# Kernel tuning notes

Hardware: AMD Instinct MI355X
Metric: run time of the kernel (lower is better)

Reference implementation:

```python
import jax, jax.numpy as jnp
import numpy as np

M_DIM = 1024
H_DIM = 1024
NEG = -1e9


def setup_inputs() -> dict:
    key = jax.random.key(0)
    ks = jax.random.split(key, 9)
    B, S = 4, 2048
    q = jax.random.normal(ks[0], (B, S, M_DIM), dtype=jnp.float32)
    k = jax.random.normal(ks[1], (B, S, M_DIM), dtype=jnp.float32)
    v = jax.random.normal(ks[2], (B, S, M_DIM), dtype=jnp.float32)
    attention_mask = jnp.ones((B, S), dtype=jnp.int32)
    sc = 1.0 / np.sqrt(M_DIM)
    Wq_w = jax.random.normal(ks[3], (H_DIM, M_DIM), dtype=jnp.float32) * sc
    Wq_b = jnp.zeros((H_DIM,), dtype=jnp.float32)
    Wk_w = jax.random.normal(ks[4], (H_DIM, M_DIM), dtype=jnp.float32) * sc
    Wk_b = jnp.zeros((H_DIM,), dtype=jnp.float32)
    Wv_w = jax.random.normal(ks[5], (H_DIM, M_DIM), dtype=jnp.float32) * sc
    Wv_b = jnp.zeros((H_DIM,), dtype=jnp.float32)
    return {"q": q, "k": k, "v": v, "attention_mask": attention_mask,
            "Wq_w": Wq_w, "Wq_b": Wq_b, "Wk_w": Wk_w, "Wk_b": Wk_b,
            "Wv_w": Wv_w, "Wv_b": Wv_b}


def reference(q, k, v, attention_mask, Wq_w, Wq_b, Wk_w, Wk_b, Wv_w, Wv_b):
    # Linear projections (torch Linear: x @ W.T + b)
    qh = jnp.einsum('bsm,hm->bsh', q, Wq_w) + Wq_b
    kh = jnp.einsum('bsm,hm->bsh', k, Wk_w) + Wk_b
    vh = jnp.einsum('bsm,hm->bsh', v, Wv_w) + Wv_b
    # Scaled dot-product scores: [B, Sq, Sk]
    scores = jnp.einsum('bqh,bkh->bqk', qh, kh) / jnp.sqrt(jnp.float32(H_DIM))
    # Padding mask: attention_mask [B, Sk] -> [B, 1, Sk]
    pad = attention_mask.astype(bool)[:, None, :]
    scores = jnp.where(pad, scores, NEG)
    # Causal mask (apply_mask=True)
    Sq, Sk = scores.shape[1], scores.shape[2]
    causal = jnp.tril(jnp.ones((Sq, Sk), dtype=bool))
    scores = jnp.where(causal[None, :, :], scores, NEG)
    attn = jax.nn.softmax(scores, axis=-1)
    out = jnp.einsum('bqk,bkh->bqh', attn, vh)
    # dropout is identity in eval mode
    return out
```

## Files before the change

### kernel.cpp

```cpp
#include <hip/hip_runtime.h>
#include <stdint.h>


typedef __attribute__((ext_vector_type(8))) short s8v;
typedef __attribute__((ext_vector_type(4))) float f4v;

__device__ __forceinline__ unsigned short f2bf(float f) {
    union { float f; unsigned u; } v; v.f = f;
    unsigned u = v.u;
    u = u + 0x7fffu + ((u >> 16) & 1u);
    return (unsigned short)(u >> 16);
}

__device__ __forceinline__ void gld_lds16(const void* gptr, void* lptr) {
    __builtin_amdgcn_global_load_lds(
        (const __attribute__((address_space(1))) unsigned int*)(uintptr_t)gptr,
        (__attribute__((address_space(3))) unsigned int*)(unsigned int)(uintptr_t)lptr,
        16, 0, 0);
}

__global__ __launch_bounds__(256) void convert_all(
    const float* __restrict__ q, const float* __restrict__ k, const float* __restrict__ v,
    const float* __restrict__ wq, const float* __restrict__ wk, const float* __restrict__ wv,
    unsigned short* __restrict__ qb, unsigned short* __restrict__ kb, unsigned short* __restrict__ vb,
    unsigned short* __restrict__ wqb, unsigned short* __restrict__ wkb, unsigned short* __restrict__ wvb,
    float* __restrict__ l)
{
    int b = blockIdx.x;
    if (b >= 27648) {
        int li = (b - 27648) * 256 + threadIdx.x;
        l[li] = 0.f;
        return;
    }
    const float* src; unsigned short* dst; int blk;
    if (b < 8192)       { src = q;  dst = qb;  blk = b; }
    else if (b < 16384) { src = k;  dst = kb;  blk = b - 8192; }
    else if (b < 24576) { src = v;  dst = vb;  blk = b - 16384; }
    else if (b < 25600) { src = wq; dst = wqb; blk = b - 24576; }
    else if (b < 26624) { src = wk; dst = wkb; blk = b - 25600; }
    else                { src = wv; dst = wvb; blk = b - 26624; }
    size_t idx = (size_t)blk * 1024 + (size_t)threadIdx.x * 4;
    float4 f = *(const float4*)(src + idx);
    ushort4 o = make_ushort4(f2bf(f.x), f2bf(f.y), f2bf(f.z), f2bf(f.w));
    *(ushort4*)(dst + idx) = o;
}

__device__ __forceinline__ void gemm_tiles(
    const unsigned short* __restrict__ A, int lda,
    const unsigned short* __restrict__ Bt, int ldb,
    int m0, int n0, int kTiles,
    unsigned short* As, unsigned short* Bs,
    f4v acc[4][4])
{
    const int t    = threadIdx.x;
    const int lane = t & 63;
    const int wave = t >> 6;
    const int wm   = (wave >> 1) * 64;
    const int wn   = (wave & 1) * 64;
    const int l15  = lane & 15;
    const int quad = lane >> 4;

    const int c0 = t, c1 = t + 256;
    unsigned short* As0 = As + (c0 & ~63) * 8;
    unsigned short* As1 = As + (c1 & ~63) * 8;
    unsigned short* Bs0 = Bs + (c0 & ~63) * 8;
    unsigned short* Bs1 = Bs + (c1 & ~63) * 8;
    const unsigned short* Ag0 = A  + (size_t)(m0 + (c0 >> 2)) * lda + (c0 & 3) * 8;
    const unsigned short* Ag1 = A  + (size_t)(m0 + (c1 >> 2)) * lda + (c1 & 3) * 8;
    const unsigned short* Bg0 = Bt + (size_t)(n0 + (c0 >> 2)) * ldb + (c0 & 3) * 8;
    const unsigned short* Bg1 = Bt + (size_t)(n0 + (c1 >> 2)) * ldb + (c1 & 3) * 8;

    const unsigned short* a_base = As + quad * 8;
    const unsigned short* b_base = Bs + quad * 8;

    gld_lds16(Ag0, As0);
    gld_lds16(Ag1, As1);
    gld_lds16(Bg0, Bs0);
    gld_lds16(Bg1, Bs1);

    for (int kt = 0; kt < kTiles; ++kt) {
        __syncthreads();
        Ag0 += 32; Ag1 += 32; Bg0 += 32; Bg1 += 32;
        if (kt + 1 < kTiles) {
            const int nb = ((kt + 1) & 1) * 4096;
            gld_lds16(Ag0, As0 + nb);
            gld_lds16(Ag1, As1 + nb);
            gld_lds16(Bg0, Bs0 + nb);
            gld_lds16(Bg1, Bs1 + nb);
        }
        const int cb = (kt & 1) * 4096;
        s8v af[4], bf[4];
        #pragma unroll
        for (int i = 0; i < 4; ++i)
            af[i] = *(const s8v*)(a_base + cb + (wm + i * 16 + l15) * 32);
        #pragma unroll
        for (int j = 0; j < 4; ++j)
            bf[j] = *(const s8v*)(b_base + cb + (wn + j * 16 + l15) * 32);
        #pragma unroll
        for (int i = 0; i < 4; ++i)
            #pragma unroll
            for (int j = 0; j < 4; ++j)
                acc[i][j] = __builtin_amdgcn_mfma_f32_16x16x32_bf16(af[i], bf[j], acc[i][j], 0, 0, 0);
    }
}

#define ACC_INIT  f4v acc[4][4]; { f4v z = {0.f,0.f,0.f,0.f}; \
    _Pragma("unroll") for (int i = 0; i < 4; ++i) \
    _Pragma("unroll") for (int j = 0; j < 4; ++j) acc[i][j] = z; }

#define LANE_VARS \
    const int lane = threadIdx.x & 63; const int wave = threadIdx.x >> 6; \
    const int wm = (wave >> 1) * 64;  const int wn = (wave & 1) * 64; \
    const int l15 = lane & 15;        const int quad = lane >> 4;

__global__ __launch_bounds__(256) void proj_kernel(
    const unsigned short* __restrict__ qb, const unsigned short* __restrict__ wqb,
    const float* __restrict__ bq, unsigned short* __restrict__ QH,
    const unsigned short* __restrict__ kb, const unsigned short* __restrict__ wkb,
    const float* __restrict__ bk, unsigned short* __restrict__ KH,
    const unsigned short* __restrict__ vb, const unsigned short* __restrict__ wvb,
    const float* __restrict__ bv, unsigned short* __restrict__ VHT)
{
    const int z = blockIdx.z;
    const unsigned short* X; const unsigned short* W; const float* bias; unsigned short* Y;
    if (z == 0)      { X = qb; W = wqb; bias = bq; Y = QH; }
    else if (z == 1) { X = kb; W = wkb; bias = bk; Y = KH; }
    else             { X = vb; W = wvb; bias = bv; Y = VHT; }

    __shared__ __align__(16) unsigned short As[2 * 128 * 32];
    __shared__ __align__(16) unsigned short Bs[2 * 128 * 32];
    const int m0 = blockIdx.x * 128;
    const int n0 = blockIdx.y * 128;
    ACC_INIT;
    gemm_tiles(X, 1024, W, 1024, m0, n0, 32, As, Bs, acc);
    LANE_VARS;
    #pragma unroll
    for (int i = 0; i < 4; ++i) {
        int row = m0 + wm + i * 16 + quad * 4;
        #pragma unroll
        for (int j = 0; j < 4; ++j) {
            int col = n0 + wn + j * 16 + l15;
            float bvv = bias[col];
            if (z != 2) {
                #pragma unroll
                for (int r = 0; r < 4; ++r)
                    Y[(size_t)(row + r) * 1024 + col] = f2bf(acc[i][j][r] + bvv);
            } else {
                int bb = row >> 11;
                int s  = row & 2047;
                ushort4 o = make_ushort4(f2bf(acc[i][j][0] + bvv), f2bf(acc[i][j][1] + bvv),
                                         f2bf(acc[i][j][2] + bvv), f2bf(acc[i][j][3] + bvv));
                *(ushort4*)(Y + (size_t)bb * (1024 * 2048) + (size_t)col * 2048 + s) = o;
            }
        }
    }
}

__global__ __launch_bounds__(256) void score_kernel(
    const unsigned short* __restrict__ QH, const unsigned short* __restrict__ KH,
    const int* __restrict__ mask, unsigned short* __restrict__ P, float* __restrict__ lsum)
{
    const int b = blockIdx.y;
    int tq = blockIdx.x;
    int qt = 0;
    while ((qt + 1) * (qt + 2) / 2 <= tq) ++qt;
    const int kt = tq - qt * (qt + 1) / 2;

    __shared__ __align__(16) unsigned short As[2 * 128 * 32];
    __shared__ __align__(16) unsigned short Bs[2 * 128 * 32];
    const unsigned short* A  = QH + (size_t)b * 2048 * 1024;
    const unsigned short* Bt = KH + (size_t)b * 2048 * 1024;
    unsigned short* Pb = P + (size_t)b * 2048 * 2048;
    float* lb = lsum + b * 2048;
    const int* mb = mask + b * 2048;
    const int m0 = qt * 128, n0 = kt * 128;
    ACC_INIT;
    gemm_tiles(A, 1024, Bt, 1024, m0, n0, 32, As, Bs, acc);
    LANE_VARS;
    float rs[4][4];
    #pragma unroll
    for (int i = 0; i < 4; ++i)
        #pragma unroll
        for (int r = 0; r < 4; ++r) rs[i][r] = 0.f;
    #pragma unroll
    for (int i = 0; i < 4; ++i) {
        int qbase = m0 + wm + i * 16 + quad * 4;
        #pragma unroll
        for (int j = 0; j < 4; ++j) {
            int kg = n0 + wn + j * 16 + l15;
            int mv = mb[kg];
            #pragma unroll
            for (int r = 0; r < 4; ++r) {
                float s = acc[i][j][r] * 0.03125f;
                float p = (mv && (kg <= qbase + r)) ? __expf(s) : 0.f;
                Pb[(size_t)(qbase + r) * 2048 + kg] = f2bf(p);
                rs[i][r] += p;
            }
        }
    }
    #pragma unroll
    for (int i = 0; i < 4; ++i)
        #pragma unroll
        for (int r = 0; r < 4; ++r) {
            float v_ = rs[i][r];
            v_ += __shfl_xor(v_, 1);
            v_ += __shfl_xor(v_, 2);
            v_ += __shfl_xor(v_, 4);
            v_ += __shfl_xor(v_, 8);
            if (l15 == 0)
                atomicAdd(&lb[m0 + wm + i * 16 + quad * 4 + r], v_);
        }
}

__constant__ int pv_qt[24] = {15,15, 7,14,14,13,13, 6,12,12,11,11, 5,10,10, 9, 9, 4, 8, 8, 3, 2, 1, 0};
__constant__ int pv_ks[24] = { 0,32, 0, 0,30, 0,28, 0, 0,26, 0,24, 0, 0,22, 0,20, 0, 0,18, 0, 0, 0, 0};
__constant__ int pv_kc[24] = {32,32,32,30,30,28,28,28,26,26,24,24,24,22,22,20,20,20,18,18,16,12, 8, 4};

__global__ __launch_bounds__(256) void pv_kernel(
    const unsigned short* __restrict__ P, const unsigned short* __restrict__ VHT,
    const float* __restrict__ lsum, float* __restrict__ Out, float* __restrict__ Part)
{
    const int nt = blockIdx.x, y = blockIdx.y, b = blockIdx.z;
    const int qt = pv_qt[y], kstart = pv_ks[y], kcount = pv_kc[y];

    __shared__ __align__(16) unsigned short As[2 * 128 * 32];
    __shared__ __align__(16) unsigned short Bs[2 * 128 * 32];
    const unsigned short* A  = P   + (size_t)b * 2048 * 2048 + (size_t)kstart * 32;
    const unsigned short* Bt = VHT + (size_t)b * 1024 * 2048 + (size_t)kstart * 32;
    const float* lb = lsum + b * 2048;
    const int m0 = qt * 128, n0 = nt * 128;
    ACC_INIT;
    gemm_tiles(A, 2048, Bt, 2048, m0, n0, kcount, As, Bs, acc);
    LANE_VARS;
    float* dst; int rowoff;
    if (kstart == 0) { dst = Out  + (size_t)b * 2048 * 1024; rowoff = 0; }
    else             { dst = Part + (size_t)b * 1024 * 1024; rowoff = -1024; }
    #pragma unroll
    for (int i = 0; i < 4; ++i) {
        int q0 = m0 + wm + i * 16 + quad * 4;
        float inv[4];
        #pragma unroll
        for (int r = 0; r < 4; ++r) inv[r] = 1.0f / lb[q0 + r];
        #pragma unroll
        for (int j = 0; j < 4; ++j) {
            int h = n0 + wn + j * 16 + l15;
            #pragma unroll
            for (int r = 0; r < 4; ++r)
                dst[(size_t)(q0 + r + rowoff) * 1024 + h] = acc[i][j][r] * inv[r];
        }
    }
}

__global__ __launch_bounds__(256) void add_partial(
    float4* __restrict__ Out4, const float4* __restrict__ Part4)
{
    int i = blockIdx.x * 256 + threadIdx.x;
    int b = i >> 18;
    int rem = i & 262143;
    int oi = b * 524288 + 262144 + rem;
    float4 o = Out4[oi], p = Part4[i];
    o.x += p.x; o.y += p.y; o.z += p.z; o.w += p.w;
    Out4[oi] = o;
}

extern "C" void kernel_launch(void* const* d_in, const int* in_sizes, int n_in,
                              void* d_out, int out_size, void* d_ws, size_t ws_size,
                              hipStream_t stream)
{
    const float* q    = (const float*)d_in[0];
    const float* k    = (const float*)d_in[1];
    const float* v    = (const float*)d_in[2];
    const int*   mask = (const int*)d_in[3];
    const float* Wq   = (const float*)d_in[4];
    const float* bq   = (const float*)d_in[5];
    const float* Wk   = (const float*)d_in[6];
    const float* bk   = (const float*)d_in[7];
    const float* Wv   = (const float*)d_in[8];
    const float* bv   = (const float*)d_in[9];
    float* out = (float*)d_out;

    char* ws = (char*)d_ws;
    size_t off = 0;
    auto take = [&](size_t bytes) { char* p = ws + off; off += (bytes + 255) & ~(size_t)255; return p; };
    unsigned short* qb  = (unsigned short*)take(8192ull * 1024 * 2);
    unsigned short* kb  = (unsigned short*)take(8192ull * 1024 * 2);
    unsigned short* vb  = (unsigned short*)take(8192ull * 1024 * 2);
    unsigned short* wqb = (unsigned short*)take(1024ull * 1024 * 2);
    unsigned short* wkb = (unsigned short*)take(1024ull * 1024 * 2);
    unsigned short* wvb = (unsigned short*)take(1024ull * 1024 * 2);
    unsigned short* QH  = (unsigned short*)take(8192ull * 1024 * 2);
    unsigned short* KH  = (unsigned short*)take(8192ull * 1024 * 2);
    unsigned short* VHT = (unsigned short*)take(8192ull * 1024 * 2);
    unsigned short* P   = (unsigned short*)take(4ull * 2048 * 2048 * 2);
    float*          l   = (float*)take(4ull * 2048 * 4);
    float*          Part = (float*)qb;

    convert_all<<<27680, 256, 0, stream>>>(q, k, v, Wq, Wk, Wv,
                                           qb, kb, vb, wqb, wkb, wvb, l);
    proj_kernel<<<dim3(64, 8, 3), 256, 0, stream>>>(qb, wqb, bq, QH,
                                                    kb, wkb, bk, KH,
                                                    vb, wvb, bv, VHT);
    score_kernel<<<dim3(136, 4), 256, 0, stream>>>(QH, KH, mask, P, l);
    pv_kernel<<<dim3(8, 24, 4), 256, 0, stream>>>(P, VHT, l, out, Part);
    add_partial<<<4096, 256, 0, stream>>>((float4*)out, (const float4*)Part);
}
```

Before: 316.2 us.

## Replace split-K partial buffer with atomic accumulation and unroll GEMM double-buffer loop

The PV kernel's split-K blocks for the lower half of the query rows now atomically add into the output, which the convert kernel zeroes beforehand. This removes the Part buffer and the separate add_partial kernel launch. The shared GEMM loop is also manually unrolled by two with fixed buffer parities and 32-bit offsets, to cut per-iteration address arithmetic. In exchange, float atomics add contention on the output and make the summation order nondeterministic, and the unrolled loop assumes kTiles is even.

```diff
diff --git a/kernel.cpp b/kernel.cpp
--- a/kernel.cpp
+++ b/kernel.cpp
@@ -24,9 +24,16 @@
     const float* __restrict__ wq, const float* __restrict__ wk, const float* __restrict__ wv,
     unsigned short* __restrict__ qb, unsigned short* __restrict__ kb, unsigned short* __restrict__ vb,
     unsigned short* __restrict__ wqb, unsigned short* __restrict__ wkb, unsigned short* __restrict__ wvb,
-    float* __restrict__ l)
+    float* __restrict__ l, float4* __restrict__ Out4)
 {
     int b = blockIdx.x;
+    if (b >= 27680) {
+        int i = (b - 27680) * 256 + threadIdx.x;
+        int bb = i >> 18;
+        int rem = i & 262143;
+        Out4[bb * 524288 + 262144 + rem] = make_float4(0.f, 0.f, 0.f, 0.f);
+        return;
+    }
     if (b >= 27648) {
         int li = (b - 27648) * 256 + threadIdx.x;
         l[li] = 0.f;
@@ -65,42 +72,47 @@
     unsigned short* As1 = As + (c1 & ~63) * 8;
     unsigned short* Bs0 = Bs + (c0 & ~63) * 8;
     unsigned short* Bs1 = Bs + (c1 & ~63) * 8;
-    const unsigned short* Ag0 = A  + (size_t)(m0 + (c0 >> 2)) * lda + (c0 & 3) * 8;
-    const unsigned short* Ag1 = A  + (size_t)(m0 + (c1 >> 2)) * lda + (c1 & 3) * 8;
-    const unsigned short* Bg0 = Bt + (size_t)(n0 + (c0 >> 2)) * ldb + (c0 & 3) * 8;
-    const unsigned short* Bg1 = Bt + (size_t)(n0 + (c1 >> 2)) * ldb + (c1 & 3) * 8;
+    const unsigned aoff0 = (unsigned)(m0 + (c0 >> 2)) * lda + (c0 & 3) * 8;
+    const unsigned aoff1 = (unsigned)(m0 + (c1 >> 2)) * lda + (c1 & 3) * 8;
+    const unsigned boff0 = (unsigned)(n0 + (c0 >> 2)) * ldb + (c0 & 3) * 8;
+    const unsigned boff1 = (unsigned)(n0 + (c1 >> 2)) * ldb + (c1 & 3) * 8;
 
     const unsigned short* a_base = As + quad * 8;
     const unsigned short* b_base = Bs + quad * 8;
 
-    gld_lds16(Ag0, As0);
-    gld_lds16(Ag1, As1);
-    gld_lds16(Bg0, Bs0);
-    gld_lds16(Bg1, Bs1);
-
-    for (int kt = 0; kt < kTiles; ++kt) {
-        __syncthreads();
-        Ag0 += 32; Ag1 += 32; Bg0 += 32; Bg1 += 32;
-        if (kt + 1 < kTiles) {
-            const int nb = ((kt + 1) & 1) * 4096;
-            gld_lds16(Ag0, As0 + nb);
-            gld_lds16(Ag1, As1 + nb);
-            gld_lds16(Bg0, Bs0 + nb);
-            gld_lds16(Bg1, Bs1 + nb);
-        }
-        const int cb = (kt & 1) * 4096;
+    auto stage = [&](int kk, int par) {
+        const unsigned short* Au = A  + (size_t)kk * 32;
+        const unsigned short* Bu = Bt + (size_t)kk * 32;
+        const int pe = par * 4096;
+        gld_lds16(Au + aoff0, As0 + pe);
+        gld_lds16(Au + aoff1, As1 + pe);
+        gld_lds16(Bu + boff0, Bs0 + pe);
+        gld_lds16(Bu + boff1, Bs1 + pe);
+    };
+    auto compute = [&](int pe) {
         s8v af[4], bf[4];
         #pragma unroll
         for (int i = 0; i < 4; ++i)
-            af[i] = *(const s8v*)(a_base + cb + (wm + i * 16 + l15) * 32);
+            af[i] = *(const s8v*)(a_base + pe + (wm + i * 16 + l15) * 32);
         #pragma unroll
         for (int j = 0; j < 4; ++j)
-            bf[j] = *(const s8v*)(b_base + cb + (wn + j * 16 + l15) * 32);
+            bf[j] = *(const s8v*)(b_base + pe + (wn + j * 16 + l15) * 32);
         #pragma unroll
         for (int i = 0; i < 4; ++i)
             #pragma unroll
             for (int j = 0; j < 4; ++j)
                 acc[i][j] = __builtin_amdgcn_mfma_f32_16x16x32_bf16(af[i], bf[j], acc[i][j], 0, 0, 0);
+    };
+
+    stage(0, 0);
+    const int K2 = kTiles >> 1;
+    for (int k2 = 0; k2 < K2; ++k2) {
+        __syncthreads();
+        stage(2 * k2 + 1, 1);
+        compute(0);
+        __syncthreads();
+        if (k2 + 1 < K2) stage(2 * k2 + 2, 0);
+        compute(4096);
     }
 }
 
@@ -218,7 +230,7 @@
 
 __global__ __launch_bounds__(256) void pv_kernel(
     const unsigned short* __restrict__ P, const unsigned short* __restrict__ VHT,
-    const float* __restrict__ lsum, float* __restrict__ Out, float* __restrict__ Part)
+    const float* __restrict__ lsum, float* __restrict__ Out)
 {
     const int nt = blockIdx.x, y = blockIdx.y, b = blockIdx.z;
     const int qt = pv_qt[y], kstart = pv_ks[y], kcount = pv_kc[y];
@@ -228,13 +240,12 @@
     const unsigned short* A  = P   + (size_t)b * 2048 * 2048 + (size_t)kstart * 32;
     const unsigned short* Bt = VHT + (size_t)b * 1024 * 2048 + (size_t)kstart * 32;
     const float* lb = lsum + b * 2048;
+    float* Ob = Out + (size_t)b * 2048 * 1024;
     const int m0 = qt * 128, n0 = nt * 128;
     ACC_INIT;
     gemm_tiles(A, 2048, Bt, 2048, m0, n0, kcount, As, Bs, acc);
     LANE_VARS;
-    float* dst; int rowoff;
-    if (kstart == 0) { dst = Out  + (size_t)b * 2048 * 1024; rowoff = 0; }
-    else             { dst = Part + (size_t)b * 1024 * 1024; rowoff = -1024; }
+    const bool split = (qt >= 8);
     #pragma unroll
     for (int i = 0; i < 4; ++i) {
         int q0 = m0 + wm + i * 16 + quad * 4;
@@ -245,22 +256,13 @@
         for (int j = 0; j < 4; ++j) {
             int h = n0 + wn + j * 16 + l15;
             #pragma unroll
-            for (int r = 0; r < 4; ++r)
-                dst[(size_t)(q0 + r + rowoff) * 1024 + h] = acc[i][j][r] * inv[r];
+            for (int r = 0; r < 4; ++r) {
+                float val = acc[i][j][r] * inv[r];
+                if (split) atomicAdd(&Ob[(size_t)(q0 + r) * 1024 + h], val);
+                else       Ob[(size_t)(q0 + r) * 1024 + h] = val;
+            }
         }
     }
-}
-
-__global__ __launch_bounds__(256) void add_partial(
-    float4* __restrict__ Out4, const float4* __restrict__ Part4)
-{
-    int i = blockIdx.x * 256 + threadIdx.x;
-    int b = i >> 18;
-    int rem = i & 262143;
-    int oi = b * 524288 + 262144 + rem;
-    float4 o = Out4[oi], p = Part4[i];
-    o.x += p.x; o.y += p.y; o.z += p.z; o.w += p.w;
-    Out4[oi] = o;
 }
 
 extern "C" void kernel_launch(void* const* d_in, const int* in_sizes, int n_in,
@@ -293,14 +295,12 @@
     unsigned short* VHT = (unsigned short*)take(8192ull * 1024 * 2);
     unsigned short* P   = (unsigned short*)take(4ull * 2048 * 2048 * 2);
     float*          l   = (float*)take(4ull * 2048 * 4);
-    float*          Part = (float*)qb;
-
-    convert_all<<<27680, 256, 0, stream>>>(q, k, v, Wq, Wk, Wv,
-                                           qb, kb, vb, wqb, wkb, wvb, l);
+
+    convert_all<<<31776, 256, 0, stream>>>(q, k, v, Wq, Wk, Wv,
+                                           qb, kb, vb, wqb, wkb, wvb, l, (float4*)out);
     proj_kernel<<<dim3(64, 8, 3), 256, 0, stream>>>(qb, wqb, bq, QH,
                                                     kb, wkb, bk, KH,
                                                     vb, wvb, bv, VHT);
     score_kernel<<<dim3(136, 4), 256, 0, stream>>>(QH, KH, mask, P, l);
-    pv_kernel<<<dim3(8, 24, 4), 256, 0, stream>>>(P, VHT, l, out, Part);
-    add_partial<<<4096, 256, 0, stream>>>((float4*)out, (const float4*)Part);
-}
+    pv_kernel<<<dim3(8, 24, 4), 256, 0, stream>>>(P, VHT, l, out);
+}
```

Result: slower. 327.6 us (+3.6%).

## Swizzle LDS tile layout and unroll GEMM mainloop by two stages

Applied to the files above, without the earlier changes.

Applies an XOR swizzle to the 16-byte chunk position on both the global-to-LDS load and the fragment reads, so lanes in a quad hit different LDS banks. It also unrolls the double-buffered k-loop by two so buffer offsets are compile-time constants, and switches address math to 32-bit offsets. The unroll assumes kTiles is even, and the 32-bit offsets assume the matrices fit within 32-bit element indexing.

```diff
diff --git a/kernel.cpp b/kernel.cpp
--- a/kernel.cpp
+++ b/kernel.cpp
@@ -65,42 +65,50 @@
     unsigned short* As1 = As + (c1 & ~63) * 8;
     unsigned short* Bs0 = Bs + (c0 & ~63) * 8;
     unsigned short* Bs1 = Bs + (c1 & ~63) * 8;
-    const unsigned short* Ag0 = A  + (size_t)(m0 + (c0 >> 2)) * lda + (c0 & 3) * 8;
-    const unsigned short* Ag1 = A  + (size_t)(m0 + (c1 >> 2)) * lda + (c1 & 3) * 8;
-    const unsigned short* Bg0 = Bt + (size_t)(n0 + (c0 >> 2)) * ldb + (c0 & 3) * 8;
-    const unsigned short* Bg1 = Bt + (size_t)(n0 + (c1 >> 2)) * ldb + (c1 & 3) * 8;
-
-    const unsigned short* a_base = As + quad * 8;
-    const unsigned short* b_base = Bs + quad * 8;
-
-    gld_lds16(Ag0, As0);
-    gld_lds16(Ag1, As1);
-    gld_lds16(Bg0, Bs0);
-    gld_lds16(Bg1, Bs1);
-
-    for (int kt = 0; kt < kTiles; ++kt) {
-        __syncthreads();
-        Ag0 += 32; Ag1 += 32; Bg0 += 32; Bg1 += 32;
-        if (kt + 1 < kTiles) {
-            const int nb = ((kt + 1) & 1) * 4096;
-            gld_lds16(Ag0, As0 + nb);
-            gld_lds16(Ag1, As1 + nb);
-            gld_lds16(Bg0, Bs0 + nb);
-            gld_lds16(Bg1, Bs1 + nb);
-        }
-        const int cb = (kt & 1) * 4096;
+    const int r0 = c0 >> 2, p0 = (c0 & 3) ^ (r0 & 3);
+    const int r1 = c1 >> 2, p1 = (c1 & 3) ^ (r1 & 3);
+    const unsigned aoff0 = (unsigned)(m0 + r0) * lda + p0 * 8;
+    const unsigned aoff1 = (unsigned)(m0 + r1) * lda + p1 * 8;
+    const unsigned boff0 = (unsigned)(n0 + r0) * ldb + p0 * 8;
+    const unsigned boff1 = (unsigned)(n0 + r1) * ldb + p1 * 8;
+
+    const int swz = (quad ^ (l15 & 3)) * 8;
+    const unsigned short* a_base = As + swz;
+    const unsigned short* b_base = Bs + swz;
+
+    auto stage = [&](int kk, int par) {
+        const unsigned short* Au = A  + (size_t)kk * 32;
+        const unsigned short* Bu = Bt + (size_t)kk * 32;
+        const int pe = par * 4096;
+        gld_lds16(Au + aoff0, As0 + pe);
+        gld_lds16(Au + aoff1, As1 + pe);
+        gld_lds16(Bu + boff0, Bs0 + pe);
+        gld_lds16(Bu + boff1, Bs1 + pe);
+    };
+    auto compute = [&](int pe) {
         s8v af[4], bf[4];
         #pragma unroll
         for (int i = 0; i < 4; ++i)
-            af[i] = *(const s8v*)(a_base + cb + (wm + i * 16 + l15) * 32);
+            af[i] = *(const s8v*)(a_base + pe + (wm + i * 16 + l15) * 32);
         #pragma unroll
         for (int j = 0; j < 4; ++j)
-            bf[j] = *(const s8v*)(b_base + cb + (wn + j * 16 + l15) * 32);
+            bf[j] = *(const s8v*)(b_base + pe + (wn + j * 16 + l15) * 32);
         #pragma unroll
         for (int i = 0; i < 4; ++i)
             #pragma unroll
             for (int j = 0; j < 4; ++j)
                 acc[i][j] = __builtin_amdgcn_mfma_f32_16x16x32_bf16(af[i], bf[j], acc[i][j], 0, 0, 0);
+    };
+
+    stage(0, 0);
+    const int K2 = kTiles >> 1;
+    for (int k2 = 0; k2 < K2; ++k2) {
+        __syncthreads();
+        stage(2 * k2 + 1, 1);
+        compute(0);
+        __syncthreads();
+        if (k2 + 1 < K2) stage(2 * k2 + 2, 0);
+        compute(4096);
     }
 }
 
```

Result: no change. 318.3 us (+0.7%).
